# Optimization experiments

Measured on AMD Instinct MI355X. Metric: run time of the kernel, lower is better.

Reference implementation:

```python
import jax, jax.numpy as jnp
import numpy as np

B, S, D, H, DFF = 4, 1024, 1024, 16, 4096
MAX_LEN = 1024
DK = D // H
EPS = 1e-5


def _ln(x, g, b):
    m = jnp.mean(x, axis=-1, keepdims=True)
    v = jnp.mean(jnp.square(x - m), axis=-1, keepdims=True)
    return (x - m) / jnp.sqrt(v + EPS) * g + b


def setup_inputs() -> dict:
    key = jax.random.key(0)
    ks = jax.random.split(key, 16)
    s = 0.02
    inp = {
        "x": jax.random.normal(ks[0], (B, S, D), jnp.float32),
        "wq": jax.random.normal(ks[1], (D, D), jnp.float32) * s,
        "bq": jnp.zeros((D,), jnp.float32),
        "wk": jax.random.normal(ks[2], (D, D), jnp.float32) * s,
        "bk": jnp.zeros((D,), jnp.float32),
        "wv": jax.random.normal(ks[3], (D, D), jnp.float32) * s,
        "bv": jnp.zeros((D,), jnp.float32),
        "wo": jax.random.normal(ks[4], (D, D), jnp.float32) * s,
        "bo": jnp.zeros((D,), jnp.float32),
        "rel_table": jax.random.normal(ks[5], (2 * MAX_LEN - 1, H), jnp.float32) * s,
        "ln1_g": jnp.ones((D,), jnp.float32),
        "ln1_b": jnp.zeros((D,), jnp.float32),
        "w1": jax.random.normal(ks[6], (D, DFF), jnp.float32) * s,
        "b1": jnp.zeros((DFF,), jnp.float32),
        "w2": jax.random.normal(ks[7], (DFF, D), jnp.float32) * s,
        "b2": jnp.zeros((D,), jnp.float32),
        "ln2_g": jnp.ones((D,), jnp.float32),
        "ln2_b": jnp.zeros((D,), jnp.float32),
        "mask": jnp.ones((B, 1, 1, S), jnp.int32),
    }
    return inp


def reference(x, wq, bq, wk, bk, wv, bv, wo, bo, rel_table,
              ln1_g, ln1_b, w1, b1, w2, b2, ln2_g, ln2_b, mask):
    # --- multi-head attention with relative position bias (post-LN encoder layer, eval mode) ---
    q = (x @ wq + bq).reshape(B, S, H, DK).transpose(0, 2, 1, 3)  # [B,H,S,dk]
    k = (x @ wk + bk).reshape(B, S, H, DK).transpose(0, 2, 1, 3)
    v = (x @ wv + bv).reshape(B, S, H, DK).transpose(0, 2, 1, 3)

    scores = jnp.einsum('bhqd,bhkd->bhqk', q, k) / jnp.sqrt(jnp.float32(DK))

    # relative position bias: table[(q - k + max_len - 1).clip] -> [1,H,S,S]
    coords = jnp.arange(S)[:, None] - jnp.arange(S)[None, :] + (MAX_LEN - 1)
    coords = jnp.clip(coords, 0, 2 * MAX_LEN - 2)
    bias = rel_table[coords]              # [S,S,H]
    scores = scores + bias.transpose(2, 0, 1)[None]

    scores = jnp.where(mask == 0, jnp.float32(-1e9), scores)
    attn = jax.nn.softmax(scores, axis=-1)
    ctx = jnp.einsum('bhqk,bhkd->bhqd', attn, v)
    ctx = ctx.transpose(0, 2, 1, 3).reshape(B, S, D)
    attn_out = ctx @ wo + bo

    x1 = _ln(x + attn_out, ln1_g, ln1_b)

    ff = jax.nn.relu(x1 @ w1 + b1) @ w2 + b2
    return _ln(x1 + ff, ln2_g, ln2_b)
```

## Files before the change

kernel.cpp:

```cpp
#include <hip/hip_runtime.h>
#include <hip/hip_bf16.h>

typedef __hip_bfloat16 bf16;
typedef __attribute__((ext_vector_type(8))) short short8;
typedef __attribute__((ext_vector_type(4))) float f32x4;

#define LOG2E 1.4426950408889634f

typedef const __attribute__((address_space(1))) void* gptr_t;
typedef __attribute__((address_space(3))) void* sptr_t;

__device__ __forceinline__ void async16(void* lds, const void* g) {
  __builtin_amdgcn_global_load_lds((gptr_t)g, (sptr_t)lds, 16, 0, 0);
}

__device__ __forceinline__ float bf2f(unsigned short u) {
  union { unsigned int i; float f; } c; c.i = ((unsigned int)u) << 16; return c.f;
}


__global__ __launch_bounds__(256) void cast_f2b_kernel(
    const float* __restrict__ src, bf16* __restrict__ dst, int n) {
  int i = (blockIdx.x * 256 + threadIdx.x) * 4;
  if (i >= n) return;
  float4 v = *(const float4*)(src + i);
  bf16 h4[4] = {__float2bfloat16(v.x), __float2bfloat16(v.y),
                __float2bfloat16(v.z), __float2bfloat16(v.w)};
  *(uint2*)((unsigned short*)dst + i) = *(uint2*)h4;
}

__global__ __launch_bounds__(256) void concat_bias(
    const float* __restrict__ bq, const float* __restrict__ bk,
    const float* __restrict__ bv, float* __restrict__ o) {
  int i = blockIdx.x * 256 + threadIdx.x;
  if (i >= 3072) return;
  o[i] = (i < 1024) ? bq[i] : (i < 2048 ? bk[i - 1024] : bv[i - 2048]);
}

__global__ __launch_bounds__(256) void transpose_all(
    const float* __restrict__ wq, const float* __restrict__ wk,
    const float* __restrict__ wv, const float* __restrict__ wo,
    const float* __restrict__ w1, const float* __restrict__ w2,
    bf16* __restrict__ dqkv, bf16* __restrict__ dwo,
    bf16* __restrict__ dw1, bf16* __restrict__ dw2) {
  __shared__ float tl[32][33];
  const int bid = blockIdx.x;
  const float* s;
  bf16* d;
  int NN, KK, n0, k0;
  if (bid < 4096) {
    int m = bid >> 10, tile = bid & 1023;
    s = m == 0 ? wq : m == 1 ? wk : m == 2 ? wv : wo;
    d = m < 3 ? dqkv + (size_t)m * 1024 * 1024 : dwo;
    NN = 1024; KK = 1024;
    n0 = (tile & 31) * 32; k0 = (tile >> 5) * 32;
  } else if (bid < 8192) {
    int tile = bid - 4096;
    s = w1; d = dw1; NN = 4096; KK = 1024;
    n0 = (tile & 127) * 32; k0 = (tile >> 7) * 32;
  } else {
    int tile = bid - 8192;
    s = w2; d = dw2; NN = 1024; KK = 4096;
    n0 = (tile & 31) * 32; k0 = (tile >> 5) * 32;
  }
  const int tx = threadIdx.x & 31, ty = threadIdx.x >> 5;
#pragma unroll
  for (int j = 0; j < 4; ++j)
    tl[ty + j * 8][tx] = s[(size_t)(k0 + ty + j * 8) * NN + n0 + tx];
  __syncthreads();
#pragma unroll
  for (int j = 0; j < 4; ++j)
    d[(size_t)(n0 + ty + j * 8) * KK + k0 + tx] =
        __float2bfloat16(tl[tx][ty + j * 8]);
}

__global__ __launch_bounds__(256) void build_vt(
    const bf16* __restrict__ qkv, bf16* __restrict__ vt) {
  __shared__ bf16 tl[32][33];
  const int bhz = blockIdx.z, s0 = blockIdx.x * 32, dk0 = blockIdx.y * 32;
  const int b = bhz >> 4, h = bhz & 15;
  const int tx = threadIdx.x, ty = threadIdx.y;
#pragma unroll
  for (int j = 0; j < 4; ++j) {
    int s = s0 + ty + j * 8;
    tl[ty + j * 8][tx] =
        qkv[(size_t)(b * 1024 + s) * 3072 + 2048 + h * 64 + dk0 + tx];
  }
  __syncthreads();
#pragma unroll
  for (int j = 0; j < 4; ++j) {
    int dk = dk0 + ty + j * 8;
    vt[(size_t)(bhz * 64 + dk) * 1024 + s0 + tx] = tl[tx][ty + j * 8];
  }
}


template <int RELU>
__global__ __launch_bounds__(256) void gemm_bt(
    const bf16* __restrict__ A, const bf16* __restrict__ Bt,
    const float* __restrict__ bias, bf16* __restrict__ C, int M, int N, int K) {
  __shared__ bf16 As[128 * 64];
  __shared__ bf16 Bs[128 * 64];
  const int t = threadIdx.x;
  const int w = t >> 6, l = t & 63;
  const int m0 = blockIdx.y * 128, n0 = blockIdx.x * 128;
  const int wr = (w >> 1) * 64, wc = (w & 1) * 64;
  const int srow = l >> 3, scol = l & 7;
  const int lm = l & 15, lq = l >> 4;

  f32x4 acc[4][4];
#pragma unroll
  for (int i = 0; i < 4; ++i)
#pragma unroll
    for (int j = 0; j < 4; ++j) acc[i][j] = (f32x4){0.f, 0.f, 0.f, 0.f};

  auto stage = [&](int k0) {
#pragma unroll
    for (int p = 0; p < 4; ++p) {
      int row = p * 32 + w * 8 + srow;
      int gc = scol ^ (row & 7);
      async16(&As[(p * 32 + w * 8) * 64], A + (size_t)(m0 + row) * K + k0 + gc * 8);
      async16(&Bs[(p * 32 + w * 8) * 64], Bt + (size_t)(n0 + row) * K + k0 + gc * 8);
    }
  };

  stage(0);
  const int niter = K >> 6;
  for (int it = 0; it < niter; ++it) {
    __syncthreads();
    short8 af[2][4], bfr[2][4];
#pragma unroll
    for (int kk = 0; kk < 2; ++kk)
#pragma unroll
      for (int mi = 0; mi < 4; ++mi) {
        int rowa = wr + mi * 16 + lm;
        af[kk][mi] = *(const short8*)&As[rowa * 64 + (((kk * 4 + lq) ^ (rowa & 7)) << 3)];
        int rowb = wc + mi * 16 + lm;
        bfr[kk][mi] = *(const short8*)&Bs[rowb * 64 + (((kk * 4 + lq) ^ (rowb & 7)) << 3)];
      }
    __syncthreads();
    if (it + 1 < niter) stage((it + 1) << 6);
#pragma unroll
    for (int kk = 0; kk < 2; ++kk)
#pragma unroll
      for (int mi = 0; mi < 4; ++mi)
#pragma unroll
        for (int ni = 0; ni < 4; ++ni)
          acc[mi][ni] = __builtin_amdgcn_mfma_f32_16x16x32_bf16(
              af[kk][mi], bfr[kk][ni], acc[mi][ni], 0, 0, 0);
  }
#pragma unroll
  for (int mi = 0; mi < 4; ++mi)
#pragma unroll
    for (int r = 0; r < 4; ++r) {
      int row = m0 + wr + mi * 16 + lq * 4 + r;
#pragma unroll
      for (int ni = 0; ni < 4; ++ni) {
        int col = n0 + wc + ni * 16 + lm;
        float v = acc[mi][ni][r] + bias[col];
        if (RELU) v = fmaxf(v, 0.f);
        C[(size_t)row * N + col] = __float2bfloat16(v);
      }
    }
}

template <typename OT>
__global__ __launch_bounds__(256) void gemm_bt_splitk(
    const bf16* __restrict__ A, const bf16* __restrict__ Bt,
    OT* __restrict__ P, int M, int N, int lda, int KS) {
  __shared__ bf16 As[128 * 64];
  __shared__ bf16 Bs[128 * 64];
  const int t = threadIdx.x;
  const int w = t >> 6, l = t & 63;
  const int m0 = blockIdx.y * 128, n0 = blockIdx.x * 128;
  const int kstart = blockIdx.z * KS;
  const int wr = (w >> 1) * 64, wc = (w & 1) * 64;
  const int srow = l >> 3, scol = l & 7;
  const int lm = l & 15, lq = l >> 4;

  f32x4 acc[4][4];
#pragma unroll
  for (int i = 0; i < 4; ++i)
#pragma unroll
    for (int j = 0; j < 4; ++j) acc[i][j] = (f32x4){0.f, 0.f, 0.f, 0.f};

  auto stage = [&](int k0) {
#pragma unroll
    for (int p = 0; p < 4; ++p) {
      int row = p * 32 + w * 8 + srow;
      int gc = scol ^ (row & 7);
      async16(&As[(p * 32 + w * 8) * 64], A + (size_t)(m0 + row) * lda + k0 + gc * 8);
      async16(&Bs[(p * 32 + w * 8) * 64], Bt + (size_t)(n0 + row) * lda + k0 + gc * 8);
    }
  };

  stage(kstart);
  const int niter = KS >> 6;
  for (int it = 0; it < niter; ++it) {
    __syncthreads();
    short8 af[2][4], bfr[2][4];
#pragma unroll
    for (int kk = 0; kk < 2; ++kk)
#pragma unroll
      for (int mi = 0; mi < 4; ++mi) {
        int rowa = wr + mi * 16 + lm;
        af[kk][mi] = *(const short8*)&As[rowa * 64 + (((kk * 4 + lq) ^ (rowa & 7)) << 3)];
        int rowb = wc + mi * 16 + lm;
        bfr[kk][mi] = *(const short8*)&Bs[rowb * 64 + (((kk * 4 + lq) ^ (rowb & 7)) << 3)];
      }
    __syncthreads();
    if (it + 1 < niter) stage(kstart + ((it + 1) << 6));
#pragma unroll
    for (int kk = 0; kk < 2; ++kk)
#pragma unroll
      for (int mi = 0; mi < 4; ++mi)
#pragma unroll
        for (int ni = 0; ni < 4; ++ni)
          acc[mi][ni] = __builtin_amdgcn_mfma_f32_16x16x32_bf16(
              af[kk][mi], bfr[kk][ni], acc[mi][ni], 0, 0, 0);
  }
  OT* Pz = P + (size_t)blockIdx.z * M * N;
#pragma unroll
  for (int mi = 0; mi < 4; ++mi)
#pragma unroll
    for (int r = 0; r < 4; ++r) {
      int row = m0 + wr + mi * 16 + lq * 4 + r;
#pragma unroll
      for (int ni = 0; ni < 4; ++ni) {
        int col = n0 + wc + ni * 16 + lm;
        float v = acc[mi][ni][r];
        if constexpr (sizeof(OT) == 4)
          Pz[(size_t)row * N + col] = v;
        else
          Pz[(size_t)row * N + col] = __float2bfloat16(v);
      }
    }
}


__global__ __launch_bounds__(512, 4) void flash_attn(
    const bf16* __restrict__ qkv, const bf16* __restrict__ vt,
    const float* __restrict__ rel, const int* __restrict__ mask,
    bf16* __restrict__ ctx) {
  __shared__ bf16 Kl[2][64 * 64];
  __shared__ bf16 Vl[2][64 * 64];
  __shared__ bf16 Pl[128 * 64];
  __shared__ float bias_s[2][192];
  __shared__ float mask_s[2][64];

  const int t = threadIdx.x;
  const int w = t >> 6, l = t & 63;
  const int lm = l & 15, lq = l >> 4;
  const int qt = blockIdx.x, bh = blockIdx.y;
  const int b = bh >> 4, h = bh & 15;
  const int q0 = qt * 128;
  const int srow = l >> 3;
  const int gc = (l & 7) ^ srow;
  const int qq = w * 16 + lm;

  auto stage = [&](int d, int k0n) {
    async16(&Kl[d][w * 8 * 64],
            qkv + (size_t)(b * 1024 + k0n + w * 8 + srow) * 3072 + 1024 + h * 64 + gc * 8);
    async16(&Vl[d][w * 8 * 64],
            vt + ((size_t)bh * 64 + w * 8 + srow) * 1024 + k0n + gc * 8);
    if (t < 191) bias_s[d][t] = rel[(q0 - k0n + 960 + t) * 16 + h] * LOG2E;
    if (t < 64) mask_s[d][t] = (mask[b * 1024 + k0n + t] == 0) ? -1.44e9f : 0.f;
  };

#pragma unroll
  for (int p = 0; p < 2; ++p)
    async16(&Pl[(p * 64 + w * 8) * 64],
            qkv + (size_t)(b * 1024 + q0 + p * 64 + w * 8 + srow) * 3072 + h * 64 + gc * 8);
  stage(0, 0);
  __syncthreads();

  short8 qf[2];
#pragma unroll
  for (int kk = 0; kk < 2; ++kk)
    qf[kk] = *(const short8*)&Pl[qq * 64 + (((kk * 4 + lq) ^ (lm & 7)) << 3)];
  __syncthreads();

  float m_st = -1e30f, l_st = 0.f;
  f32x4 acc_o[4];
#pragma unroll
  for (int j = 0; j < 4; ++j) acc_o[j] = (f32x4){0.f, 0.f, 0.f, 0.f};

  const float C0 = 0.125f * LOG2E;

  for (int kt = 0; kt < 16; ++kt) {
    const int d = kt & 1;
    if (kt < 15) stage(d ^ 1, (kt + 1) * 64);

    f32x4 sa[4];
#pragma unroll
    for (int i = 0; i < 4; ++i) sa[i] = (f32x4){0.f, 0.f, 0.f, 0.f};
#pragma unroll
    for (int kk = 0; kk < 2; ++kk) {
      short8 ak[4];
#pragma unroll
      for (int mi = 0; mi < 4; ++mi) {
        int row = mi * 16 + lm;
        ak[mi] = *(const short8*)&Kl[d][row * 64 + (((kk * 4 + lq) ^ (lm & 7)) << 3)];
      }
#pragma unroll
      for (int mi = 0; mi < 4; ++mi)
        sa[mi] = __builtin_amdgcn_mfma_f32_16x16x32_bf16(ak[mi], qf[kk], sa[mi], 0, 0, 0);
    }

    float m4[4][4];
#pragma unroll
    for (int mi = 0; mi < 4; ++mi)
      *(float4*)m4[mi] = *(const float4*)&mask_s[d][mi * 16 + lq * 4];
    float mx = -1e30f;
#pragma unroll
    for (int mi = 0; mi < 4; ++mi)
#pragma unroll
      for (int r = 0; r < 4; ++r) {
        int kl = mi * 16 + lq * 4 + r;
        float v = sa[mi][r] * C0 + (bias_s[d][qq - kl + 63] + m4[mi][r]);
        sa[mi][r] = v;
        mx = fmaxf(mx, v);
      }
    mx = fmaxf(mx, __shfl_xor(mx, 16));
    mx = fmaxf(mx, __shfl_xor(mx, 32));
    float mn = fmaxf(m_st, mx);
    float alpha = __builtin_amdgcn_exp2f(m_st - mn);
    m_st = mn;
    float ls = 0.f;
#pragma unroll
    for (int mi = 0; mi < 4; ++mi)
#pragma unroll
      for (int r = 0; r < 4; ++r) {
        float p = __builtin_amdgcn_exp2f(sa[mi][r] - mn);
        sa[mi][r] = p;
        ls += p;
      }
    ls += __shfl_xor(ls, 16);
    ls += __shfl_xor(ls, 32);
    l_st = l_st * alpha + ls;

#pragma unroll
    for (int mi = 0; mi < 4; ++mi) {
      bf16 h4[4];
#pragma unroll
      for (int r = 0; r < 4; ++r) h4[r] = __float2bfloat16(sa[mi][r]);
      int chunk = mi * 2 + (lq >> 1);
      *(uint2*)&Pl[qq * 64 + ((chunk ^ (lm & 7)) << 3) + ((lq & 1) << 2)] =
          *(uint2*)h4;
    }

#pragma unroll
    for (int r = 0; r < 4; ++r) {
      float a = __shfl(alpha, lq * 4 + r);
#pragma unroll
      for (int ni = 0; ni < 4; ++ni) acc_o[ni][r] *= a;
    }

#pragma unroll
    for (int kk2 = 0; kk2 < 2; ++kk2) {
      short8 pf = *(const short8*)&Pl[qq * 64 + (((kk2 * 4 + lq) ^ (lm & 7)) << 3)];
      short8 vf[4];
#pragma unroll
      for (int ni = 0; ni < 4; ++ni) {
        int rowv = ni * 16 + lm;
        vf[ni] = *(const short8*)&Vl[d][rowv * 64 + (((kk2 * 4 + lq) ^ (lm & 7)) << 3)];
      }
#pragma unroll
      for (int ni = 0; ni < 4; ++ni)
        acc_o[ni] = __builtin_amdgcn_mfma_f32_16x16x32_bf16(pf, vf[ni], acc_o[ni], 0, 0, 0);
    }
    __syncthreads();
  }

  float linv = 1.f / l_st;
#pragma unroll
  for (int r = 0; r < 4; ++r) {
    float il = __shfl(linv, lq * 4 + r);
    int qx = w * 16 + lq * 4 + r;
    size_t rowbase = (size_t)(b * 1024 + q0 + qx) * 1024 + h * 64;
#pragma unroll
    for (int ni = 0; ni < 4; ++ni)
      ctx[rowbase + ni * 16 + lm] = __float2bfloat16(acc_o[ni][r] * il);
  }
}


template <typename PT, int NS>
__global__ __launch_bounds__(256) void ln_resid(
    const float* __restrict__ xin, const PT* __restrict__ part,
    const float* __restrict__ bias,
    const float* __restrict__ gw, const float* __restrict__ bw,
    float* __restrict__ outf, bf16* __restrict__ outb) {
  const int row = blockIdx.x, t = threadIdx.x;
  const size_t base = (size_t)row * 1024 + t * 4;
  float4 xv = *(const float4*)(xin + base);
  float4 bi = *(const float4*)(bias + t * 4);
  float v0 = xv.x + bi.x, v1 = xv.y + bi.y, v2 = xv.z + bi.z, v3 = xv.w + bi.w;
#pragma unroll
  for (int s = 0; s < NS; ++s) {
    const PT* p = part + (size_t)s * 4194304 + base;
    if constexpr (sizeof(PT) == 4) {
      float4 pv = *(const float4*)p;
      v0 += pv.x; v1 += pv.y; v2 += pv.z; v3 += pv.w;
    } else {
      ushort4 pv = *(const ushort4*)p;
      v0 += bf2f(pv.x); v1 += bf2f(pv.y); v2 += bf2f(pv.z); v3 += bf2f(pv.w);
    }
  }
  float s1 = v0 + v1 + v2 + v3;
  float s2 = v0 * v0 + v1 * v1 + v2 * v2 + v3 * v3;
#pragma unroll
  for (int o = 1; o < 64; o <<= 1) {
    s1 += __shfl_xor(s1, o);
    s2 += __shfl_xor(s2, o);
  }
  __shared__ float red[8];
  const int w = t >> 6, l = t & 63;
  if (l == 0) { red[w] = s1; red[4 + w] = s2; }
  __syncthreads();
  float S1 = red[0] + red[1] + red[2] + red[3];
  float S2 = red[4] + red[5] + red[6] + red[7];
  float mean = S1 * (1.f / 1024.f);
  float var = S2 * (1.f / 1024.f) - mean * mean;
  float rstd = rsqrtf(var + 1e-5f);
  float4 gv = *(const float4*)(gw + t * 4);
  float4 bv = *(const float4*)(bw + t * 4);
  float o0 = (v0 - mean) * rstd * gv.x + bv.x;
  float o1 = (v1 - mean) * rstd * gv.y + bv.y;
  float o2 = (v2 - mean) * rstd * gv.z + bv.z;
  float o3 = (v3 - mean) * rstd * gv.w + bv.w;
  if (outf) {
    float4 ov = {o0, o1, o2, o3};
    *(float4*)(outf + base) = ov;
  }
  if (outb) {
    bf16 h4[4] = {__float2bfloat16(o0), __float2bfloat16(o1),
                  __float2bfloat16(o2), __float2bfloat16(o3)};
    *(uint2*)((unsigned short*)outb + base) = *(uint2*)h4;
  }
}


extern "C" void kernel_launch(void* const* d_in, const int* in_sizes, int n_in,
                              void* d_out, int out_size, void* d_ws, size_t ws_size,
                              hipStream_t stream) {
  (void)in_sizes; (void)n_in; (void)out_size; (void)ws_size;
  const float* x   = (const float*)d_in[0];
  const float* wq  = (const float*)d_in[1];
  const float* bq  = (const float*)d_in[2];
  const float* wk  = (const float*)d_in[3];
  const float* bk  = (const float*)d_in[4];
  const float* wv  = (const float*)d_in[5];
  const float* bv  = (const float*)d_in[6];
  const float* wo  = (const float*)d_in[7];
  const float* bo  = (const float*)d_in[8];
  const float* rel = (const float*)d_in[9];
  const float* g1  = (const float*)d_in[10];
  const float* be1 = (const float*)d_in[11];
  const float* w1  = (const float*)d_in[12];
  const float* b1  = (const float*)d_in[13];
  const float* w2  = (const float*)d_in[14];
  const float* b2  = (const float*)d_in[15];
  const float* g2  = (const float*)d_in[16];
  const float* be2 = (const float*)d_in[17];
  const int* mask  = (const int*)d_in[18];
  float* out = (float*)d_out;

  char* ws = (char*)d_ws;
  bf16*  xb      = (bf16*)(ws + 0);
  bf16*  wqkv_t  = (bf16*)(ws + 8388608);
  bf16*  wo_t    = (bf16*)(ws + 14680064);
  bf16*  w1_t    = (bf16*)(ws + 16777216);
  bf16*  ctx_b   = (bf16*)(ws + 25165824);
  bf16*  x1b     = (bf16*)(ws + 33554432);
  bf16*  qkv_b   = (bf16*)(ws + 41943040);
  bf16*  vtb     = (bf16*)(ws + 67108864);
  bf16*  part_wo = (bf16*)(ws + 41943040);
  bf16*  h1      = (bf16*)(ws + 41943040);
  bf16*  part_ff = (bf16*)(ws + 0);
  bf16*  w2_t    = (bf16*)(ws + 75497472);
  float* x1f     = (float*)(ws + 83886080);
  float* bqkv    = (float*)(ws + 100663296);

  dim3 tb(32, 8);
  cast_f2b_kernel<<<4096, 256, 0, stream>>>(x, xb, 4096 * 1024);
  concat_bias<<<12, 256, 0, stream>>>(bq, bk, bv, bqkv);
  transpose_all<<<12288, 256, 0, stream>>>(
      wq, wk, wv, wo, w1, w2, wqkv_t, wo_t, w1_t, w2_t);

  gemm_bt<0><<<dim3(24, 32), 256, 0, stream>>>(xb, wqkv_t, bqkv, qkv_b, 4096, 3072, 1024);
  build_vt<<<dim3(32, 2, 64), tb, 0, stream>>>(qkv_b, vtb);
  flash_attn<<<dim3(8, 64), 512, 0, stream>>>(qkv_b, vtb, rel, mask, ctx_b);
  gemm_bt_splitk<bf16><<<dim3(8, 32, 2), 256, 0, stream>>>(
      ctx_b, wo_t, part_wo, 4096, 1024, 1024, 512);
  ln_resid<bf16, 2><<<4096, 256, 0, stream>>>(x, part_wo, bo, g1, be1, x1f, x1b);
  gemm_bt<1><<<dim3(32, 32), 256, 0, stream>>>(x1b, w1_t, b1, h1, 4096, 4096, 1024);
  gemm_bt_splitk<bf16><<<dim3(8, 32, 4), 256, 0, stream>>>(
      h1, w2_t, part_ff, 4096, 1024, 4096, 1024);
  ln_resid<bf16, 4><<<4096, 256, 0, stream>>>(x1f, part_ff, b2, g2, be2, out, nullptr);
}
```

Measured before the change: 341.4 us.

## Double-buffer GEMM LDS tiles, merge prep kernels, halve FFN2 split-K

Both GEMM kernels now keep two LDS buffers. The next K-tile loads asynchronously into the other buffer, which removes the second barrier per iteration and lets loads overlap the MFMA work. The three preprocessing kernels (x cast, bias concat, weight transposes) become one launch. The FFN2 split-K factor drops from 4 to 2, which halves the partial-sum traffic and the reduction work in the LayerNorm step. The trade-offs are doubled LDS use per block, which may cut occupancy, and fewer blocks for FFN2.

```diff
diff --git a/kernel.cpp b/kernel.cpp
--- a/kernel.cpp
+++ b/kernel.cpp
@@ -19,47 +19,49 @@
 }
 
 
-__global__ __launch_bounds__(256) void cast_f2b_kernel(
-    const float* __restrict__ src, bf16* __restrict__ dst, int n) {
-  int i = (blockIdx.x * 256 + threadIdx.x) * 4;
-  if (i >= n) return;
-  float4 v = *(const float4*)(src + i);
-  bf16 h4[4] = {__float2bfloat16(v.x), __float2bfloat16(v.y),
-                __float2bfloat16(v.z), __float2bfloat16(v.w)};
-  *(uint2*)((unsigned short*)dst + i) = *(uint2*)h4;
-}
-
-__global__ __launch_bounds__(256) void concat_bias(
-    const float* __restrict__ bq, const float* __restrict__ bk,
-    const float* __restrict__ bv, float* __restrict__ o) {
-  int i = blockIdx.x * 256 + threadIdx.x;
-  if (i >= 3072) return;
-  o[i] = (i < 1024) ? bq[i] : (i < 2048 ? bk[i - 1024] : bv[i - 2048]);
-}
-
-__global__ __launch_bounds__(256) void transpose_all(
+__global__ __launch_bounds__(256) void prep_all(
+    const float* __restrict__ x, const float* __restrict__ bq,
+    const float* __restrict__ bk, const float* __restrict__ bv,
     const float* __restrict__ wq, const float* __restrict__ wk,
     const float* __restrict__ wv, const float* __restrict__ wo,
     const float* __restrict__ w1, const float* __restrict__ w2,
+    bf16* __restrict__ xb, float* __restrict__ bqkv,
     bf16* __restrict__ dqkv, bf16* __restrict__ dwo,
     bf16* __restrict__ dw1, bf16* __restrict__ dw2) {
+  const int bid = blockIdx.x;
+  if (bid < 4096) {
+    int i = (bid * 256 + threadIdx.x) * 4;
+    float4 v = *(const float4*)(x + i);
+    bf16 h4[4] = {__float2bfloat16(v.x), __float2bfloat16(v.y),
+                  __float2bfloat16(v.z), __float2bfloat16(v.w)};
+    *(uint2*)((unsigned short*)xb + i) = *(uint2*)h4;
+    return;
+  }
+  if (bid == 16384) {
+#pragma unroll
+    for (int j = 0; j < 12; ++j) {
+      int i = j * 256 + threadIdx.x;
+      bqkv[i] = (i < 1024) ? bq[i] : (i < 2048 ? bk[i - 1024] : bv[i - 2048]);
+    }
+    return;
+  }
   __shared__ float tl[32][33];
-  const int bid = blockIdx.x;
+  const int tid = bid - 4096;
   const float* s;
   bf16* d;
   int NN, KK, n0, k0;
-  if (bid < 4096) {
-    int m = bid >> 10, tile = bid & 1023;
+  if (tid < 4096) {
+    int m = tid >> 10, tile = tid & 1023;
     s = m == 0 ? wq : m == 1 ? wk : m == 2 ? wv : wo;
     d = m < 3 ? dqkv + (size_t)m * 1024 * 1024 : dwo;
     NN = 1024; KK = 1024;
     n0 = (tile & 31) * 32; k0 = (tile >> 5) * 32;
-  } else if (bid < 8192) {
-    int tile = bid - 4096;
+  } else if (tid < 8192) {
+    int tile = tid - 4096;
     s = w1; d = dw1; NN = 4096; KK = 1024;
     n0 = (tile & 127) * 32; k0 = (tile >> 7) * 32;
   } else {
-    int tile = bid - 8192;
+    int tile = tid - 8192;
     s = w2; d = dw2; NN = 1024; KK = 4096;
     n0 = (tile & 31) * 32; k0 = (tile >> 5) * 32;
   }
@@ -99,8 +101,8 @@
 __global__ __launch_bounds__(256) void gemm_bt(
     const bf16* __restrict__ A, const bf16* __restrict__ Bt,
     const float* __restrict__ bias, bf16* __restrict__ C, int M, int N, int K) {
-  __shared__ bf16 As[128 * 64];
-  __shared__ bf16 Bs[128 * 64];
+  __shared__ bf16 As[2][128 * 64];
+  __shared__ bf16 Bs[2][128 * 64];
   const int t = threadIdx.x;
   const int w = t >> 6, l = t & 63;
   const int m0 = blockIdx.y * 128, n0 = blockIdx.x * 128;
@@ -114,19 +116,20 @@
 #pragma unroll
     for (int j = 0; j < 4; ++j) acc[i][j] = (f32x4){0.f, 0.f, 0.f, 0.f};
 
-  auto stage = [&](int k0) {
+  auto stage = [&](int k0, int d) {
 #pragma unroll
     for (int p = 0; p < 4; ++p) {
       int row = p * 32 + w * 8 + srow;
       int gc = scol ^ (row & 7);
-      async16(&As[(p * 32 + w * 8) * 64], A + (size_t)(m0 + row) * K + k0 + gc * 8);
-      async16(&Bs[(p * 32 + w * 8) * 64], Bt + (size_t)(n0 + row) * K + k0 + gc * 8);
+      async16(&As[d][(p * 32 + w * 8) * 64], A + (size_t)(m0 + row) * K + k0 + gc * 8);
+      async16(&Bs[d][(p * 32 + w * 8) * 64], Bt + (size_t)(n0 + row) * K + k0 + gc * 8);
     }
   };
 
-  stage(0);
+  stage(0, 0);
   const int niter = K >> 6;
   for (int it = 0; it < niter; ++it) {
+    const int d = it & 1;
     __syncthreads();
     short8 af[2][4], bfr[2][4];
 #pragma unroll
@@ -134,12 +137,11 @@
 #pragma unroll
       for (int mi = 0; mi < 4; ++mi) {
         int rowa = wr + mi * 16 + lm;
-        af[kk][mi] = *(const short8*)&As[rowa * 64 + (((kk * 4 + lq) ^ (rowa & 7)) << 3)];
+        af[kk][mi] = *(const short8*)&As[d][rowa * 64 + (((kk * 4 + lq) ^ (rowa & 7)) << 3)];
         int rowb = wc + mi * 16 + lm;
-        bfr[kk][mi] = *(const short8*)&Bs[rowb * 64 + (((kk * 4 + lq) ^ (rowb & 7)) << 3)];
-      }
-    __syncthreads();
-    if (it + 1 < niter) stage((it + 1) << 6);
+        bfr[kk][mi] = *(const short8*)&Bs[d][rowb * 64 + (((kk * 4 + lq) ^ (rowb & 7)) << 3)];
+      }
+    if (it + 1 < niter) stage((it + 1) << 6, d ^ 1);
 #pragma unroll
     for (int kk = 0; kk < 2; ++kk)
 #pragma unroll
@@ -168,8 +170,8 @@
 __global__ __launch_bounds__(256) void gemm_bt_splitk(
     const bf16* __restrict__ A, const bf16* __restrict__ Bt,
     OT* __restrict__ P, int M, int N, int lda, int KS) {
-  __shared__ bf16 As[128 * 64];
-  __shared__ bf16 Bs[128 * 64];
+  __shared__ bf16 As[2][128 * 64];
+  __shared__ bf16 Bs[2][128 * 64];
   const int t = threadIdx.x;
   const int w = t >> 6, l = t & 63;
   const int m0 = blockIdx.y * 128, n0 = blockIdx.x * 128;
@@ -184,19 +186,20 @@
 #pragma unroll
     for (int j = 0; j < 4; ++j) acc[i][j] = (f32x4){0.f, 0.f, 0.f, 0.f};
 
-  auto stage = [&](int k0) {
+  auto stage = [&](int k0, int d) {
 #pragma unroll
     for (int p = 0; p < 4; ++p) {
       int row = p * 32 + w * 8 + srow;
       int gc = scol ^ (row & 7);
-      async16(&As[(p * 32 + w * 8) * 64], A + (size_t)(m0 + row) * lda + k0 + gc * 8);
-      async16(&Bs[(p * 32 + w * 8) * 64], Bt + (size_t)(n0 + row) * lda + k0 + gc * 8);
+      async16(&As[d][(p * 32 + w * 8) * 64], A + (size_t)(m0 + row) * lda + k0 + gc * 8);
+      async16(&Bs[d][(p * 32 + w * 8) * 64], Bt + (size_t)(n0 + row) * lda + k0 + gc * 8);
     }
   };
 
-  stage(kstart);
+  stage(kstart, 0);
   const int niter = KS >> 6;
   for (int it = 0; it < niter; ++it) {
+    const int d = it & 1;
     __syncthreads();
     short8 af[2][4], bfr[2][4];
 #pragma unroll
@@ -204,12 +207,11 @@
 #pragma unroll
       for (int mi = 0; mi < 4; ++mi) {
         int rowa = wr + mi * 16 + lm;
-        af[kk][mi] = *(const short8*)&As[rowa * 64 + (((kk * 4 + lq) ^ (rowa & 7)) << 3)];
+        af[kk][mi] = *(const short8*)&As[d][rowa * 64 + (((kk * 4 + lq) ^ (rowa & 7)) << 3)];
         int rowb = wc + mi * 16 + lm;
-        bfr[kk][mi] = *(const short8*)&Bs[rowb * 64 + (((kk * 4 + lq) ^ (rowb & 7)) << 3)];
-      }
-    __syncthreads();
-    if (it + 1 < niter) stage(kstart + ((it + 1) << 6));
+        bfr[kk][mi] = *(const short8*)&Bs[d][rowb * 64 + (((kk * 4 + lq) ^ (rowb & 7)) << 3)];
+      }
+    if (it + 1 < niter) stage(kstart + ((it + 1) << 6), d ^ 1);
 #pragma unroll
     for (int kk = 0; kk < 2; ++kk)
 #pragma unroll
@@ -483,10 +485,8 @@
   float* bqkv    = (float*)(ws + 100663296);
 
   dim3 tb(32, 8);
-  cast_f2b_kernel<<<4096, 256, 0, stream>>>(x, xb, 4096 * 1024);
-  concat_bias<<<12, 256, 0, stream>>>(bq, bk, bv, bqkv);
-  transpose_all<<<12288, 256, 0, stream>>>(
-      wq, wk, wv, wo, w1, w2, wqkv_t, wo_t, w1_t, w2_t);
+  prep_all<<<16385, 256, 0, stream>>>(x, bq, bk, bv, wq, wk, wv, wo, w1, w2,
+                                      xb, bqkv, wqkv_t, wo_t, w1_t, w2_t);
 
   gemm_bt<0><<<dim3(24, 32), 256, 0, stream>>>(xb, wqkv_t, bqkv, qkv_b, 4096, 3072, 1024);
   build_vt<<<dim3(32, 2, 64), tb, 0, stream>>>(qkv_b, vtb);
@@ -495,7 +495,7 @@
       ctx_b, wo_t, part_wo, 4096, 1024, 1024, 512);
   ln_resid<bf16, 2><<<4096, 256, 0, stream>>>(x, part_wo, bo, g1, be1, x1f, x1b);
   gemm_bt<1><<<dim3(32, 32), 256, 0, stream>>>(x1b, w1_t, b1, h1, 4096, 4096, 1024);
-  gemm_bt_splitk<bf16><<<dim3(8, 32, 4), 256, 0, stream>>>(
-      h1, w2_t, part_ff, 4096, 1024, 4096, 1024);
-  ln_resid<bf16, 4><<<4096, 256, 0, stream>>>(x1f, part_ff, b2, g2, be2, out, nullptr);
-}
+  gemm_bt_splitk<bf16><<<dim3(8, 32, 2), 256, 0, stream>>>(
+      h1, w2_t, part_ff, 4096, 1024, 4096, 2048);
+  ln_resid<bf16, 2><<<4096, 256, 0, stream>>>(x1f, part_ff, b2, g2, be2, out, nullptr);
+}
```

After: 324.1 us. 1.05x faster.
